# Performance work log

Measured on AMD Instinct MI355X. Metric: run time of the kernel, lower is better.

## Reference

```python
import jax, jax.numpy as jnp
import numpy as np

EMBED = 256
HEADS = 8
N, L, S = 4, 128, 64


def setup_inputs() -> dict:
    key = jax.random.key(0)
    ks = jax.random.split(key, 9)
    values = jax.random.normal(ks[0], (N, L, S, EMBED), dtype=jnp.float32)
    keys_ = jax.random.normal(ks[1], (N, L, S, EMBED), dtype=jnp.float32)
    query = jax.random.normal(ks[2], (N, L, S, EMBED), dtype=jnp.float32)
    mask = jax.random.randint(ks[3], (N, 1, L, L, 1), 0, 2, dtype=jnp.int32)
    sc = 1.0 / np.sqrt(EMBED)
    Wq = jax.random.normal(ks[4], (EMBED, EMBED), dtype=jnp.float32) * sc
    Wk = jax.random.normal(ks[5], (EMBED, EMBED), dtype=jnp.float32) * sc
    Wv = jax.random.normal(ks[6], (EMBED, EMBED), dtype=jnp.float32) * sc
    Wo = jax.random.normal(ks[7], (HEADS * EMBED, EMBED), dtype=jnp.float32) * (1.0 / np.sqrt(HEADS * EMBED))
    bo = jnp.zeros((EMBED,), dtype=jnp.float32)
    return {"values": values, "keys": keys_, "query": query, "mask": mask,
            "Wq": Wq, "Wk": Wk, "Wv": Wv, "Wo": Wo, "bo": bo}


def reference(values, keys, query, mask, Wq, Wk, Wv, Wo, bo):
    n, q_len, s_len, d = query.shape
    k_len = keys.shape[1]
    h = HEADS
    # Per-head projections share one weight (expand happens BEFORE Linear in
    # the original), so compute each projection once and broadcast over heads.
    q = jnp.einsum('nqsd,de->nqse', query, Wq)   # [N,Q,S,D]
    k = jnp.einsum('nksd,de->nkse', keys, Wk)    # [N,K,S,D]
    v = jnp.einsum('nksd,de->nkse', values, Wv)  # [N,K,S,D]
    # energy: nqshd,nkshd->nhqks ; identical across h pre-mask
    energy = jnp.einsum('nqsd,nksd->nqks', q, k)            # [N,Q,K,S]
    energy = jnp.broadcast_to(energy[:, None], (n, h, q_len, k_len, s_len))
    energy = jnp.where(mask == 0, jnp.float32(-1e20), energy)
    attn = jax.nn.softmax(energy / jnp.sqrt(jnp.float32(d)), axis=3)  # over K
    # out: nhqls,nlshd->nqshd
    out = jnp.einsum('nhqks,nksd->nqshd', attn, v)
    out = out.reshape(n, q_len, s_len, h * d)
    return out @ Wo + bo
```

## Files before the change

### kernel.cpp

```cpp
#include <hip/hip_runtime.h>
#include <hip/hip_bf16.h>


using bf16x4 = __attribute__((ext_vector_type(4))) __bf16;
using bf16x8 = __attribute__((ext_vector_type(8))) __bf16;
using f32x4  = __attribute__((ext_vector_type(4))) float;

#define MFMA(a, b, c) __builtin_amdgcn_mfma_f32_16x16x32_bf16((a), (b), (c), 0, 0, 0)

__global__ __launch_bounds__(256) void prep_pack(
    const float* __restrict__ Wq, const float* __restrict__ Wk,
    const float* __restrict__ Wv, const float* __restrict__ Wo,
    __bf16* __restrict__ wqp, __bf16* __restrict__ wkp,
    __bf16* __restrict__ wvp, __bf16* __restrict__ wop) {
  int idx = blockIdx.x * 256 + threadIdx.x;
  int j = idx & 7, lane = (idx >> 3) & 63, k8 = (idx >> 9) & 7, ct = idx >> 12;
  int e = ct * 16 + (lane & 15);
  int d = k8 * 32 + (lane >> 4) * 8 + j;
  wqp[idx] = (__bf16)Wq[d * 256 + e];
  wkp[idx] = (__bf16)Wk[d * 256 + e];
  wvp[idx] = (__bf16)Wv[d * 256 + e];
  float s = 0.f;
#pragma unroll
  for (int h = 0; h < 8; ++h) s += Wo[(h * 256 + d) * 256 + e];
  wop[idx] = (__bf16)s;
}

__global__ __launch_bounds__(512) void fused_attn(
    const float* __restrict__ Xv, const float* __restrict__ Xk,
    const float* __restrict__ Xq, const int* __restrict__ mask,
    const __bf16* __restrict__ wqp, const __bf16* __restrict__ wkp,
    const __bf16* __restrict__ wvp, const __bf16* __restrict__ wop,
    const float* __restrict__ bo, float* __restrict__ out) {
  extern __shared__ char lds[];
  char* Areg = lds;
  char* Breg = lds + 65536;
  char* Creg = lds + 131072;
  const int t = threadIdx.x, lane = t & 63, w = t >> 6;
  const int lr = lane & 15, g = lane >> 4;
  const int sl = blockIdx.x, n = sl >> 6, s = sl & 63;

  auto stageX = [&](const float* __restrict__ X) {
#pragma unroll
    for (int i = 0; i < 16; ++i) {
      int f = i * 512 + t;
      int row = f >> 6, c4 = f & 63;
      float4 v = *reinterpret_cast<const float4*>(
          X + ((size_t)(n * 8192 + row * 64 + s)) * 256 + c4 * 4);
      bf16x4 b; b[0]=(__bf16)v.x; b[1]=(__bf16)v.y; b[2]=(__bf16)v.z; b[3]=(__bf16)v.w;
      *reinterpret_cast<bf16x4*>(Areg + row * 512 + ((c4 * 8) ^ ((row & 7) << 4))) = b;
    }
  };
  auto projQK = [&](const __bf16* __restrict__ wpk) {
    const bf16x8* wp = reinterpret_cast<const bf16x8*>(wpk);
#pragma unroll
    for (int dth = 0; dth < 2; ++dth) {
      int dt = 2 * w + dth;
      bf16x8 wf[8];
#pragma unroll
      for (int k8 = 0; k8 < 8; ++k8) wf[k8] = wp[(dt * 8 + k8) * 64 + lane];
#pragma unroll
      for (int ct = 0; ct < 8; ++ct) {
        f32x4 acc = {0.f, 0.f, 0.f, 0.f};
#pragma unroll
        for (int k8 = 0; k8 < 8; ++k8) {
          int brow = ct * 16 + lr;
          bf16x8 xf = *reinterpret_cast<const bf16x8*>(
              Areg + brow * 512 + ((k8 * 64 + g * 16) ^ ((brow & 7) << 4)));
          acc = MFMA(wf[k8], xf, acc);
        }
        bf16x4 pb; pb[0]=(__bf16)acc[0]; pb[1]=(__bf16)acc[1];
        pb[2]=(__bf16)acc[2]; pb[3]=(__bf16)acc[3];
        *reinterpret_cast<bf16x4*>(
            Breg + ct * 8192 + w * 1024 +
            (lr + 16 * (2 * dth + (g >> 1))) * 16 + (g & 1) * 8) = pb;
      }
    }
  };
  auto projV = [&](int half, char* dest) {
    const bf16x8* wp = reinterpret_cast<const bf16x8*>(wvp);
#pragma unroll
    for (int dth = 0; dth < 2; ++dth) {
      int dt = 2 * w + dth;
      bf16x8 wf[8];
#pragma unroll
      for (int k8 = 0; k8 < 8; ++k8) wf[k8] = wp[(dt * 8 + k8) * 64 + lane];
#pragma unroll
      for (int ctl = 0; ctl < 4; ++ctl) {
        int ct = half * 4 + ctl;
        f32x4 acc = {0.f, 0.f, 0.f, 0.f};
#pragma unroll
        for (int k8 = 0; k8 < 8; ++k8) {
          int brow = ct * 16 + lr;
          bf16x8 xf = *reinterpret_cast<const bf16x8*>(
              Areg + brow * 512 + ((k8 * 64 + g * 16) ^ ((brow & 7) << 4)));
          acc = MFMA(wf[k8], xf, acc);
        }
        int kk8loc = (ct >> 1) & 1;
        char* bse = dest + (dt * 2 + kk8loc) * 1024 +
                    (16 * ((ct * 2 + (lr >> 3)) & 3)) * 16 + (lr & 7) * 2;
#pragma unroll
        for (int j = 0; j < 4; ++j)
          *reinterpret_cast<__bf16*>(bse + (4 * g + j) * 16) = (__bf16)acc[j];
      }
    }
  };

  stageX(Xq);
  __syncthreads();
  projQK(wqp);
  __syncthreads();
  bf16x8 af[8];
#pragma unroll
  for (int k8 = 0; k8 < 8; ++k8)
    af[k8] = *reinterpret_cast<const bf16x8*>(Breg + w * 8192 + k8 * 1024 + lane * 16);
  stageX(Xk);
  __syncthreads();
  projQK(wkp);
  __syncthreads();

  float4 vreg[16];
#pragma unroll
  for (int i = 0; i < 16; ++i) {
    int f = i * 512 + t;
    int row = f >> 6, c4 = f & 63;
    vreg[i] = *reinterpret_cast<const float4*>(
        Xv + ((size_t)(n * 8192 + row * 64 + s)) * 256 + c4 * 4);
  }
  int mreg[8][4];
#pragma unroll
  for (int ct = 0; ct < 8; ++ct)
#pragma unroll
    for (int j = 0; j < 4; ++j)
      mreg[ct][j] = mask[((size_t)n * 128 + w * 16 + 4 * g + j) * 128 + ct * 16 + lr];
  f32x4 sacc[8];
#pragma unroll
  for (int ct = 0; ct < 8; ++ct) {
    f32x4 a = {0.f, 0.f, 0.f, 0.f};
#pragma unroll
    for (int k8 = 0; k8 < 8; ++k8)
      a = MFMA(af[k8],
               *reinterpret_cast<const bf16x8*>(Breg + ct * 8192 + k8 * 1024 + lane * 16),
               a);
    sacc[ct] = a;
  }
#pragma unroll
  for (int i = 0; i < 16; ++i) {
    int f = i * 512 + t;
    int row = f >> 6, c4 = f & 63;
    float4 v = vreg[i];
    bf16x4 b; b[0]=(__bf16)v.x; b[1]=(__bf16)v.y; b[2]=(__bf16)v.z; b[3]=(__bf16)v.w;
    *reinterpret_cast<bf16x4*>(Areg + row * 512 + ((c4 * 8) ^ ((row & 7) << 4))) = b;
  }
  __syncthreads();

  float p[8][4];
#pragma unroll
  for (int j = 0; j < 4; ++j) {
    float mx = -3e38f;
#pragma unroll
    for (int ct = 0; ct < 8; ++ct) {
      float sv = mreg[ct][j] ? sacc[ct][j] * 0.0625f : -6.25e18f;
      p[ct][j] = sv;
      mx = fmaxf(mx, sv);
    }
#pragma unroll
    for (int o = 1; o < 16; o <<= 1) mx = fmaxf(mx, __shfl_xor(mx, o));
    float sum = 0.f;
#pragma unroll
    for (int ct = 0; ct < 8; ++ct) {
      float e = __expf(p[ct][j] - mx);
      p[ct][j] = e;
      sum += e;
    }
#pragma unroll
    for (int o = 1; o < 16; o <<= 1) sum += __shfl_xor(sum, o);
    float inv = 1.f / sum;
#pragma unroll
    for (int ct = 0; ct < 8; ++ct) p[ct][j] *= inv;
  }
#pragma unroll
  for (int ct = 0; ct < 8; ++ct) {
    char* bse = Breg + w * 4096 + (ct >> 1) * 1024 +
                (16 * ((ct * 2 + (lr >> 3)) & 3)) * 16 + (lr & 7) * 2;
#pragma unroll
    for (int j = 0; j < 4; ++j)
      *reinterpret_cast<__bf16*>(bse + (4 * g + j) * 16) = (__bf16)p[ct][j];
  }
  bf16x8 pa[4];
#pragma unroll
  for (int kk8 = 0; kk8 < 4; ++kk8)
    pa[kk8] = *reinterpret_cast<const bf16x8*>(Breg + w * 4096 + kk8 * 1024 + lane * 16);
  projV(0, Creg);
  __syncthreads();
  projV(1, Areg);
  __syncthreads();

#pragma unroll
  for (int dt = 0; dt < 16; ++dt) {
    f32x4 acc = {0.f, 0.f, 0.f, 0.f};
#pragma unroll
    for (int kk8 = 0; kk8 < 4; ++kk8) {
      const char* vb = (kk8 < 2) ? (Creg + (dt * 2 + kk8) * 1024)
                                 : (Areg + (dt * 2 + kk8 - 2) * 1024);
      acc = MFMA(pa[kk8], *reinterpret_cast<const bf16x8*>(vb + lane * 16), acc);
    }
    char* bse = Breg + w * 8192 + (dt >> 1) * 1024 +
                (16 * ((dt * 2 + (lr >> 3)) & 3)) * 16 + (lr & 7) * 2;
#pragma unroll
    for (int j = 0; j < 4; ++j)
      *reinterpret_cast<__bf16*>(bse + (4 * g + j) * 16) = (__bf16)acc[j];
  }

  bf16x8 oa[8];
#pragma unroll
  for (int k8 = 0; k8 < 8; ++k8)
    oa[k8] = *reinterpret_cast<const bf16x8*>(Breg + w * 8192 + k8 * 1024 + lane * 16);
  const bf16x8* wo = reinterpret_cast<const bf16x8*>(wop);
#pragma unroll
  for (int ct = 0; ct < 16; ++ct) {
    f32x4 acc = {0.f, 0.f, 0.f, 0.f};
#pragma unroll
    for (int k8 = 0; k8 < 8; ++k8)
      acc = MFMA(oa[k8], wo[(ct * 8 + k8) * 64 + lane], acc);
    int e = ct * 16 + lr;
    float bias = bo[e];
#pragma unroll
    for (int j = 0; j < 4; ++j) {
      int q = w * 16 + 4 * g + j;
      out[((size_t)n * 8192 + q * 64 + s) * 256 + e] = acc[j] + bias;
    }
  }
}

extern "C" void kernel_launch(void* const* d_in, const int* in_sizes, int n_in,
                              void* d_out, int out_size, void* d_ws, size_t ws_size,
                              hipStream_t stream) {
  const float* values = (const float*)d_in[0];
  const float* keys   = (const float*)d_in[1];
  const float* query  = (const float*)d_in[2];
  const int*   mask   = (const int*)d_in[3];
  const float* Wq     = (const float*)d_in[4];
  const float* Wk     = (const float*)d_in[5];
  const float* Wv     = (const float*)d_in[6];
  const float* Wo     = (const float*)d_in[7];
  const float* bo     = (const float*)d_in[8];
  float* out = (float*)d_out;

  char* w = (char*)d_ws;
  __bf16* wqp = (__bf16*)w; w += 131072;
  __bf16* wkp = (__bf16*)w; w += 131072;
  __bf16* wvp = (__bf16*)w; w += 131072;
  __bf16* wop = (__bf16*)w; w += 131072;

  prep_pack<<<256, 256, 0, stream>>>(Wq, Wk, Wv, Wo, wqp, wkp, wvp, wop);
  fused_attn<<<256, 512, 163840, stream>>>(values, keys, query, mask,
                                           wqp, wkp, wvp, wop, bo, out);
}
```

Before: 57.63 us.

## Prefetch next input into registers during projections and restructure output GEMM stores

Global loads of the next activation tensor (K, then V) are issued into registers before the current projection's MFMAs run, and converted to bf16 LDS afterwards. Each wave now computes two output column tiles that share one set of LDS activation fragments. The output projection is transposed so each lane writes float4 rows instead of scattered scalars, and launch bounds request two blocks per CU. This hides global-load latency and cuts LDS reads and store instructions, but raises register pressure. That pressure may cause spills or hold occupancy at the requested level.

```diff
diff --git a/kernel.cpp b/kernel.cpp
--- a/kernel.cpp
+++ b/kernel.cpp
@@ -26,7 +26,7 @@
   wop[idx] = (__bf16)s;
 }
 
-__global__ __launch_bounds__(512) void fused_attn(
+__global__ __launch_bounds__(512, 2) void fused_attn(
     const float* __restrict__ Xv, const float* __restrict__ Xk,
     const float* __restrict__ Xq, const int* __restrict__ mask,
     const __bf16* __restrict__ wqp, const __bf16* __restrict__ wkp,
@@ -40,93 +40,83 @@
   const int lr = lane & 15, g = lane >> 4;
   const int sl = blockIdx.x, n = sl >> 6, s = sl & 63;
 
-  auto stageX = [&](const float* __restrict__ X) {
-#pragma unroll
-    for (int i = 0; i < 16; ++i) {
-      int f = i * 512 + t;
-      int row = f >> 6, c4 = f & 63;
-      float4 v = *reinterpret_cast<const float4*>(
-          X + ((size_t)(n * 8192 + row * 64 + s)) * 256 + c4 * 4);
-      bf16x4 b; b[0]=(__bf16)v.x; b[1]=(__bf16)v.y; b[2]=(__bf16)v.z; b[3]=(__bf16)v.w;
-      *reinterpret_cast<bf16x4*>(Areg + row * 512 + ((c4 * 8) ^ ((row & 7) << 4))) = b;
+  auto fill = [&](const float* __restrict__ X, float4* vr) {
+#pragma unroll
+    for (int i = 0; i < 8; ++i) {
+      int f8 = i * 512 + t, row = f8 >> 5, c8 = f8 & 31;
+      const float* src = X + ((size_t)(n * 8192 + row * 64 + s)) * 256 + c8 * 8;
+      vr[2 * i]     = *reinterpret_cast<const float4*>(src);
+      vr[2 * i + 1] = *reinterpret_cast<const float4*>(src + 4);
     }
   };
+  auto flushv = [&](const float4* vr) {
+#pragma unroll
+    for (int i = 0; i < 8; ++i) {
+      int f8 = i * 512 + t, row = f8 >> 5, c8 = f8 & 31;
+      bf16x8 b;
+      b[0]=(__bf16)vr[2*i].x;   b[1]=(__bf16)vr[2*i].y;
+      b[2]=(__bf16)vr[2*i].z;   b[3]=(__bf16)vr[2*i].w;
+      b[4]=(__bf16)vr[2*i+1].x; b[5]=(__bf16)vr[2*i+1].y;
+      b[6]=(__bf16)vr[2*i+1].z; b[7]=(__bf16)vr[2*i+1].w;
+      *reinterpret_cast<bf16x8*>(
+          Areg + row * 512 + ((c8 * 16) ^ ((row & 7) << 4))) = b;
+    }
+  };
+
   auto projQK = [&](const __bf16* __restrict__ wpk) {
     const bf16x8* wp = reinterpret_cast<const bf16x8*>(wpk);
-#pragma unroll
-    for (int dth = 0; dth < 2; ++dth) {
-      int dt = 2 * w + dth;
-      bf16x8 wf[8];
-#pragma unroll
-      for (int k8 = 0; k8 < 8; ++k8) wf[k8] = wp[(dt * 8 + k8) * 64 + lane];
-#pragma unroll
-      for (int ct = 0; ct < 8; ++ct) {
-        f32x4 acc = {0.f, 0.f, 0.f, 0.f};
-#pragma unroll
-        for (int k8 = 0; k8 < 8; ++k8) {
-          int brow = ct * 16 + lr;
-          bf16x8 xf = *reinterpret_cast<const bf16x8*>(
-              Areg + brow * 512 + ((k8 * 64 + g * 16) ^ ((brow & 7) << 4)));
-          acc = MFMA(wf[k8], xf, acc);
-        }
-        bf16x4 pb; pb[0]=(__bf16)acc[0]; pb[1]=(__bf16)acc[1];
-        pb[2]=(__bf16)acc[2]; pb[3]=(__bf16)acc[3];
-        *reinterpret_cast<bf16x4*>(
-            Breg + ct * 8192 + w * 1024 +
-            (lr + 16 * (2 * dth + (g >> 1))) * 16 + (g & 1) * 8) = pb;
-      }
+    bf16x8 wf0[8], wf1[8];
+#pragma unroll
+    for (int k8 = 0; k8 < 8; ++k8) {
+      wf0[k8] = wp[((2 * w)     * 8 + k8) * 64 + lane];
+      wf1[k8] = wp[((2 * w + 1) * 8 + k8) * 64 + lane];
+    }
+#pragma unroll
+    for (int ct = 0; ct < 8; ++ct) {
+      bf16x8 xf[8];
+#pragma unroll
+      for (int k8 = 0; k8 < 8; ++k8) {
+        int brow = ct * 16 + lr;
+        xf[k8] = *reinterpret_cast<const bf16x8*>(
+            Areg + brow * 512 + ((k8 * 64 + g * 16) ^ ((brow & 7) << 4)));
+      }
+      f32x4 a0 = {0.f,0.f,0.f,0.f}, a1 = {0.f,0.f,0.f,0.f};
+#pragma unroll
+      for (int k8 = 0; k8 < 8; ++k8) {
+        a0 = MFMA(wf0[k8], xf[k8], a0);
+        a1 = MFMA(wf1[k8], xf[k8], a1);
+      }
+      bf16x4 p0, p1;
+#pragma unroll
+      for (int j = 0; j < 4; ++j) { p0[j] = (__bf16)a0[j]; p1[j] = (__bf16)a1[j]; }
+      *reinterpret_cast<bf16x4*>(
+          Breg + ct * 8192 + w * 1024 + (lr + 16 * (0 + (g >> 1))) * 16 + (g & 1) * 8) = p0;
+      *reinterpret_cast<bf16x4*>(
+          Breg + ct * 8192 + w * 1024 + (lr + 16 * (2 + (g >> 1))) * 16 + (g & 1) * 8) = p1;
     }
   };
-  auto projV = [&](int half, char* dest) {
-    const bf16x8* wp = reinterpret_cast<const bf16x8*>(wvp);
-#pragma unroll
-    for (int dth = 0; dth < 2; ++dth) {
-      int dt = 2 * w + dth;
-      bf16x8 wf[8];
-#pragma unroll
-      for (int k8 = 0; k8 < 8; ++k8) wf[k8] = wp[(dt * 8 + k8) * 64 + lane];
-#pragma unroll
-      for (int ctl = 0; ctl < 4; ++ctl) {
-        int ct = half * 4 + ctl;
-        f32x4 acc = {0.f, 0.f, 0.f, 0.f};
-#pragma unroll
-        for (int k8 = 0; k8 < 8; ++k8) {
-          int brow = ct * 16 + lr;
-          bf16x8 xf = *reinterpret_cast<const bf16x8*>(
-              Areg + brow * 512 + ((k8 * 64 + g * 16) ^ ((brow & 7) << 4)));
-          acc = MFMA(wf[k8], xf, acc);
-        }
-        int kk8loc = (ct >> 1) & 1;
-        char* bse = dest + (dt * 2 + kk8loc) * 1024 +
-                    (16 * ((ct * 2 + (lr >> 3)) & 3)) * 16 + (lr & 7) * 2;
-#pragma unroll
-        for (int j = 0; j < 4; ++j)
-          *reinterpret_cast<__bf16*>(bse + (4 * g + j) * 16) = (__bf16)acc[j];
-      }
-    }
-  };
-
-  stageX(Xq);
-  __syncthreads();
+
+  {
+    float4 vr[16];
+    fill(Xq, vr);
+    flushv(vr);
+  }
+  __syncthreads();
+  float4 vrp[16];
+  fill(Xk, vrp);
   projQK(wqp);
   __syncthreads();
   bf16x8 af[8];
 #pragma unroll
   for (int k8 = 0; k8 < 8; ++k8)
     af[k8] = *reinterpret_cast<const bf16x8*>(Breg + w * 8192 + k8 * 1024 + lane * 16);
-  stageX(Xk);
-  __syncthreads();
+  flushv(vrp);
+  __syncthreads();
+
+  fill(Xv, vrp);
   projQK(wkp);
   __syncthreads();
 
-  float4 vreg[16];
-#pragma unroll
-  for (int i = 0; i < 16; ++i) {
-    int f = i * 512 + t;
-    int row = f >> 6, c4 = f & 63;
-    vreg[i] = *reinterpret_cast<const float4*>(
-        Xv + ((size_t)(n * 8192 + row * 64 + s)) * 256 + c4 * 4);
-  }
   int mreg[8][4];
 #pragma unroll
   for (int ct = 0; ct < 8; ++ct)
@@ -136,22 +126,16 @@
   f32x4 sacc[8];
 #pragma unroll
   for (int ct = 0; ct < 8; ++ct) {
-    f32x4 a = {0.f, 0.f, 0.f, 0.f};
+    bf16x8 bfr[8];
 #pragma unroll
     for (int k8 = 0; k8 < 8; ++k8)
-      a = MFMA(af[k8],
-               *reinterpret_cast<const bf16x8*>(Breg + ct * 8192 + k8 * 1024 + lane * 16),
-               a);
+      bfr[k8] = *reinterpret_cast<const bf16x8*>(Breg + ct * 8192 + k8 * 1024 + lane * 16);
+    f32x4 a = {0.f,0.f,0.f,0.f};
+#pragma unroll
+    for (int k8 = 0; k8 < 8; ++k8) a = MFMA(af[k8], bfr[k8], a);
     sacc[ct] = a;
   }
-#pragma unroll
-  for (int i = 0; i < 16; ++i) {
-    int f = i * 512 + t;
-    int row = f >> 6, c4 = f & 63;
-    float4 v = vreg[i];
-    bf16x4 b; b[0]=(__bf16)v.x; b[1]=(__bf16)v.y; b[2]=(__bf16)v.z; b[3]=(__bf16)v.w;
-    *reinterpret_cast<bf16x4*>(Areg + row * 512 + ((c4 * 8) ^ ((row & 7) << 4))) = b;
-  }
+  flushv(vrp);
   __syncthreads();
 
   float p[8][4];
@@ -191,14 +175,52 @@
 #pragma unroll
   for (int kk8 = 0; kk8 < 4; ++kk8)
     pa[kk8] = *reinterpret_cast<const bf16x8*>(Breg + w * 4096 + kk8 * 1024 + lane * 16);
-  projV(0, Creg);
-  __syncthreads();
-  projV(1, Areg);
-  __syncthreads();
+
+  {
+    const bf16x8* wp = reinterpret_cast<const bf16x8*>(wvp);
+    bf16x8 vf0[8], vf1[8];
+#pragma unroll
+    for (int k8 = 0; k8 < 8; ++k8) {
+      vf0[k8] = wp[((2 * w)     * 8 + k8) * 64 + lane];
+      vf1[k8] = wp[((2 * w + 1) * 8 + k8) * 64 + lane];
+    }
+#pragma unroll
+    for (int half = 0; half < 2; ++half) {
+      char* dest = half ? Areg : Creg;
+#pragma unroll
+      for (int ctl = 0; ctl < 4; ++ctl) {
+        int ct = half * 4 + ctl;
+        bf16x8 xf[8];
+#pragma unroll
+        for (int k8 = 0; k8 < 8; ++k8) {
+          int brow = ct * 16 + lr;
+          xf[k8] = *reinterpret_cast<const bf16x8*>(
+              Areg + brow * 512 + ((k8 * 64 + g * 16) ^ ((brow & 7) << 4)));
+        }
+        f32x4 a0 = {0.f,0.f,0.f,0.f}, a1 = {0.f,0.f,0.f,0.f};
+#pragma unroll
+        for (int k8 = 0; k8 < 8; ++k8) {
+          a0 = MFMA(vf0[k8], xf[k8], a0);
+          a1 = MFMA(vf1[k8], xf[k8], a1);
+        }
+        int kk8loc = (ct >> 1) & 1;
+#pragma unroll
+        for (int dth = 0; dth < 2; ++dth) {
+          const f32x4& ac = dth ? a1 : a0;
+          char* bse = dest + ((2 * w + dth) * 2 + kk8loc) * 1024 +
+                      (16 * ((ct * 2 + (lr >> 3)) & 3)) * 16 + (lr & 7) * 2;
+#pragma unroll
+          for (int j = 0; j < 4; ++j)
+            *reinterpret_cast<__bf16*>(bse + (4 * g + j) * 16) = (__bf16)ac[j];
+        }
+      }
+      __syncthreads();
+    }
+  }
 
 #pragma unroll
   for (int dt = 0; dt < 16; ++dt) {
-    f32x4 acc = {0.f, 0.f, 0.f, 0.f};
+    f32x4 acc = {0.f,0.f,0.f,0.f};
 #pragma unroll
     for (int kk8 = 0; kk8 < 4; ++kk8) {
       const char* vb = (kk8 < 2) ? (Creg + (dt * 2 + kk8) * 1024)
@@ -211,24 +233,39 @@
     for (int j = 0; j < 4; ++j)
       *reinterpret_cast<__bf16*>(bse + (4 * g + j) * 16) = (__bf16)acc[j];
   }
-
-  bf16x8 oa[8];
-#pragma unroll
-  for (int k8 = 0; k8 < 8; ++k8)
-    oa[k8] = *reinterpret_cast<const bf16x8*>(Breg + w * 8192 + k8 * 1024 + lane * 16);
-  const bf16x8* wo = reinterpret_cast<const bf16x8*>(wop);
-#pragma unroll
-  for (int ct = 0; ct < 16; ++ct) {
-    f32x4 acc = {0.f, 0.f, 0.f, 0.f};
-#pragma unroll
-    for (int k8 = 0; k8 < 8; ++k8)
-      acc = MFMA(oa[k8], wo[(ct * 8 + k8) * 64 + lane], acc);
-    int e = ct * 16 + lr;
-    float bias = bo[e];
-#pragma unroll
-    for (int j = 0; j < 4; ++j) {
-      int q = w * 16 + 4 * g + j;
-      out[((size_t)n * 8192 + q * 64 + s) * 256 + e] = acc[j] + bias;
+  __syncthreads();
+
+  {
+    const bf16x8* wo = reinterpret_cast<const bf16x8*>(wop);
+    bf16x8 of0[8], of1[8];
+#pragma unroll
+    for (int k8 = 0; k8 < 8; ++k8) {
+      of0[k8] = wo[((2 * w)     * 8 + k8) * 64 + lane];
+      of1[k8] = wo[((2 * w + 1) * 8 + k8) * 64 + lane];
+    }
+    float4 bias0 = *reinterpret_cast<const float4*>(bo + (2 * w)     * 16 + 4 * g);
+    float4 bias1 = *reinterpret_cast<const float4*>(bo + (2 * w + 1) * 16 + 4 * g);
+#pragma unroll
+    for (int qt = 0; qt < 8; ++qt) {
+      bf16x8 bfr[8];
+#pragma unroll
+      for (int k8 = 0; k8 < 8; ++k8)
+        bfr[k8] = *reinterpret_cast<const bf16x8*>(Breg + qt * 8192 + k8 * 1024 + lane * 16);
+      f32x4 a0 = {0.f,0.f,0.f,0.f}, a1 = {0.f,0.f,0.f,0.f};
+#pragma unroll
+      for (int k8 = 0; k8 < 8; ++k8) {
+        a0 = MFMA(of0[k8], bfr[k8], a0);
+        a1 = MFMA(of1[k8], bfr[k8], a1);
+      }
+      int q = qt * 16 + lr;
+      float* orow = out + ((size_t)n * 8192 + q * 64 + s) * 256;
+      float4 o0, o1;
+      o0.x = a0[0] + bias0.x; o0.y = a0[1] + bias0.y;
+      o0.z = a0[2] + bias0.z; o0.w = a0[3] + bias0.w;
+      o1.x = a1[0] + bias1.x; o1.y = a1[1] + bias1.y;
+      o1.z = a1[2] + bias1.z; o1.w = a1[3] + bias1.w;
+      *reinterpret_cast<float4*>(orow + (2 * w)     * 16 + 4 * g) = o0;
+      *reinterpret_cast<float4*>(orow + (2 * w + 1) * 16 + 4 * g) = o1;
     }
   }
 }
```

Result: faster. 47.68 us (-17.3%).
